# Optimization experiments

Hardware: AMD Instinct MI355X
Metric: run time of the kernel (lower is better)

The kernel has to match this reference:

```python
import jax, jax.numpy as jnp
import numpy as np

D = 1152      # hidden_size
H = 16        # num_heads
DH = D // H   # head_dim = 72
NCHUNK = 8    # images
L = 1024      # tokens per image (32x32 patches)
S = NCHUNK * L


def rotate_half(x):
    x1, x2 = jnp.split(x, 2, axis=-1)
    return jnp.concatenate([-x2, x1], axis=-1)


def setup_inputs() -> dict:
    key = jax.random.key(0)
    k0, k1, k2, k3, k4 = jax.random.split(key, 5)
    hidden_states = jax.random.normal(k0, (S, D), dtype=jnp.float32)
    qkv_w = jax.random.normal(k1, (3 * D, D), dtype=jnp.float32) * 0.02
    qkv_b = jax.random.normal(k2, (3 * D,), dtype=jnp.float32) * 0.02
    proj_w = jax.random.normal(k3, (D, D), dtype=jnp.float32) * 0.02
    proj_b = jax.random.normal(k4, (D,), dtype=jnp.float32) * 0.02
    # vision RoPE tables: [S, head_dim] with duplicated half-frequencies
    pos = jnp.arange(S, dtype=jnp.float32)
    inv_freq = 1.0 / (10000.0 ** (jnp.arange(0, DH, 2, dtype=jnp.float32) / DH))
    freqs = jnp.outer(pos, inv_freq)              # [S, DH//2]
    emb = jnp.concatenate([freqs, freqs], -1)     # [S, DH]
    cos, sin = jnp.cos(emb), jnp.sin(emb)
    cu_seqlens = jnp.arange(NCHUNK + 1, dtype=jnp.int32) * L
    return dict(hidden_states=hidden_states, cos=cos, sin=sin,
                qkv_w=qkv_w, qkv_b=qkv_b, proj_w=proj_w, proj_b=proj_b,
                cu_seqlens=cu_seqlens)


def reference(hidden_states, cos, sin, qkv_w, qkv_b, proj_w, proj_b, cu_seqlens):
    seq = hidden_states.shape[0]
    num_heads = H
    head_dim = qkv_w.shape[0] // (3 * num_heads)
    # fused QKV projection (torch Linear: x @ W^T + b)
    qkv = hidden_states @ qkv_w.T + qkv_b                 # [S, 3D]
    qkv = qkv.reshape(seq, 3, num_heads, head_dim)
    q, k, v = qkv[:, 0], qkv[:, 1], qkv[:, 2]             # [S, H, DH]
    # RoPE in fp32, broadcast cos/sin over heads
    c = cos[:, None, :].astype(jnp.float32)
    s = sin[:, None, :].astype(jnp.float32)
    qf, kf = q.astype(jnp.float32), k.astype(jnp.float32)
    q = (qf * c + rotate_half(qf) * s).astype(q.dtype)
    k = (kf * c + rotate_half(kf) * s).astype(k.dtype)
    # cu_seqlens defines equal-length segments -> vectorize over chunks
    cu = np.asarray(cu_seqlens)
    chunk = int(cu[1] - cu[0])
    n = seq // chunk
    qc = q.reshape(n, chunk, num_heads, head_dim)
    kc = k.reshape(n, chunk, num_heads, head_dim)
    vc = v.reshape(n, chunk, num_heads, head_dim)
    scale = head_dim ** -0.5
    attn = jnp.einsum('nqhd,nkhd->nhqk', qc, kc) * scale  # [n,H,L,L]
    attn = jax.nn.softmax(attn.astype(jnp.float32), axis=-1).astype(q.dtype)
    out = jnp.einsum('nhqk,nkhd->nqhd', attn, vc)         # [n,L,H,DH]
    out = out.reshape(seq, num_heads * head_dim)
    return out @ proj_w.T + proj_b
```

## Files before the change

### kernel.cpp

```cpp
#include <hip/hip_runtime.h>
#include <stdint.h>

typedef unsigned short ushort_t;
typedef short bf16x8 __attribute__((ext_vector_type(8)));
typedef float f32x4 __attribute__((ext_vector_type(4)));
typedef ushort_t us2 __attribute__((ext_vector_type(2)));
typedef ushort_t us4 __attribute__((ext_vector_type(4)));
typedef ushort_t us8 __attribute__((ext_vector_type(8)));

__device__ __forceinline__ float b2f(ushort_t u) {
    union { unsigned int i; float f; } v; v.i = ((unsigned int)u) << 16; return v.f;
}
__device__ __forceinline__ ushort_t f2b(float f) {
    union { float f; unsigned int i; } v; v.f = f;
    unsigned int r = v.i + 0x7fffu + ((v.i >> 16) & 1u);
    return (ushort_t)(r >> 16);
}

typedef __attribute__((address_space(3))) unsigned int lds_u32;
typedef __attribute__((address_space(1))) const unsigned int gbl_u32;

__device__ __forceinline__ void gload_lds16(const void* g, void* l) {
    __builtin_amdgcn_global_load_lds((gbl_u32*)g, (lds_u32*)l, 16, 0, 0);
}

__global__ void cvt_f32_bf16(const float* __restrict__ src, ushort_t* __restrict__ dst, int n8)
{
    const int i = blockIdx.x * 256 + threadIdx.x;
    if (i >= n8) return;
    f32x4 a = *(const f32x4*)&src[i * 8];
    f32x4 b = *(const f32x4*)&src[i * 8 + 4];
    us8 o;
#pragma unroll
    for (int j = 0; j < 4; j++) { o[j] = f2b(a[j]); o[j + 4] = f2b(b[j]); }
    *(us8*)&dst[i * 8] = o;
}

template <bool OUT_F32>
__global__ __launch_bounds__(256, 4) void gemm_bt_bias(
    const ushort_t* __restrict__ A, const ushort_t* __restrict__ B,
    const float* __restrict__ bias, void* __restrict__ Cv,
    int M, int N, int K)
{
    __shared__ short Sm[16384];

    const int t = threadIdx.x;
    const int lane = t & 63, w = t >> 6;
    const int qd = lane >> 4, ln = lane & 15;
    const int wm = w >> 1, wn = w & 1;
    const int m0 = blockIdx.y * 128, n0 = blockIdx.x * 128;
    const int KITER = K >> 5;

    f32x4 acc[4][4];
#pragma unroll
    for (int i = 0; i < 4; i++)
#pragma unroll
        for (int j = 0; j < 4; j++) acc[i][j] = (f32x4){0.f, 0.f, 0.f, 0.f};

    const int rA = t >> 2;
    const int colSw = ((t & 3) ^ ((rA >> 1) & 3)) * 8;
    const ushort_t* gA  = A + (size_t)(m0 + rA) * K + colSw;
    const ushort_t* gA2 = A + (size_t)(m0 + 64 + rA) * K + colSw;
    const ushort_t* gB  = B + (size_t)(n0 + rA) * K + colSw;
    const ushort_t* gB2 = B + (size_t)(n0 + 64 + rA) * K + colSw;

    gload_lds16(gA,  Sm + t * 8);
    gload_lds16(gA2, Sm + (t + 256) * 8);
    gload_lds16(gB,  Sm + 8192 + t * 8);
    gload_lds16(gB2, Sm + 8192 + (t + 256) * 8);

    const int pc = (qd ^ ((ln >> 1) & 3)) * 8;

    for (int kt = 0; kt < KITER; kt++) {
        __syncthreads();
        if (kt + 1 < KITER) {
            const int k1 = (kt + 1) << 5;
            const int nbo = ((kt + 1) & 1) * 4096;
            gload_lds16(gA + k1,  Sm + nbo + t * 8);
            gload_lds16(gA2 + k1, Sm + nbo + (t + 256) * 8);
            gload_lds16(gB + k1,  Sm + 8192 + nbo + t * 8);
            gload_lds16(gB2 + k1, Sm + 8192 + nbo + (t + 256) * 8);
        }
        const int cbo = (kt & 1) * 4096;
        const short* AsB = Sm + cbo;
        const short* BsB = Sm + 8192 + cbo;

        bf16x8 af[4], bfv[4];
#pragma unroll
        for (int i = 0; i < 4; i++)
            af[i] = *(const bf16x8*)&AsB[(wm * 64 + i * 16 + ln) * 32 + pc];
#pragma unroll
        for (int j = 0; j < 4; j++)
            bfv[j] = *(const bf16x8*)&BsB[(wn * 64 + j * 16 + ln) * 32 + pc];
#pragma unroll
        for (int i = 0; i < 4; i++)
#pragma unroll
            for (int j = 0; j < 4; j++)
                acc[i][j] = __builtin_amdgcn_mfma_f32_16x16x32_bf16(
                    af[i], bfv[j], acc[i][j], 0, 0, 0);
    }

    float bv[4];
#pragma unroll
    for (int j = 0; j < 4; j++) bv[j] = bias[n0 + wn * 64 + j * 16 + ln];

    if (!OUT_F32) {
        __syncthreads();
        ushort_t* Ct = (ushort_t*)Cv;
#pragma unroll
        for (int i = 0; i < 4; i++)
#pragma unroll
            for (int j = 0; j < 4; j++)
#pragma unroll
                for (int r = 0; r < 4; r++)
                    Sm[(wm * 64 + i * 16 + qd * 4 + r) * 128 + wn * 64 + j * 16 + ln] =
                        (short)f2b(acc[i][j][r] + bv[j]);
        __syncthreads();
#pragma unroll
        for (int q = 0; q < 8; q++) {
            const int c = t + q * 256;
            const int row = c >> 4, cc = c & 15;
            *(us8*)&Ct[(size_t)(m0 + row) * N + n0 + cc * 8] =
                *(const us8*)&Sm[row * 128 + cc * 8];
        }
    } else {
        float* Ct = (float*)Cv;
        float* Cf = (float*)Sm;
#pragma unroll
        for (int p = 0; p < 2; p++) {
            __syncthreads();
            if (wm == p) {
#pragma unroll
                for (int i = 0; i < 4; i++)
#pragma unroll
                    for (int j = 0; j < 4; j++)
#pragma unroll
                        for (int r = 0; r < 4; r++)
                            Cf[(i * 16 + qd * 4 + r) * 128 + wn * 64 + j * 16 + ln] =
                                acc[i][j][r] + bv[j];
            }
            __syncthreads();
#pragma unroll
            for (int q = 0; q < 8; q++) {
                const int c = t + q * 256;
                const int row = c >> 5, cc = c & 31;
                *(f32x4*)&Ct[(size_t)(m0 + p * 64 + row) * N + n0 + cc * 4] =
                    *(const f32x4*)&Cf[row * 128 + cc * 4];
            }
        }
    }
}

__global__ void rope_qk(ushort_t* __restrict__ qkv,
                        const float* __restrict__ cosb,
                        const float* __restrict__ sinb,
                        ushort_t* __restrict__ kb)
{
    const int idx = blockIdx.x * 256 + threadIdx.x;
    const int d0c = idx % 9;
    const int h = (idx / 9) & 15;
    const int s = idx / 144;
    const int d0 = d0c * 4;
    const int n = s >> 10, l = s & 1023;
    const size_t src = (size_t)s * 3456 + h * 72;
    const size_t dstrow = ((size_t)(n * 16 + h) * 1024 + l) * 128;

    f32x4 c1 = *(const f32x4*)&cosb[s * 72 + d0];
    f32x4 c2 = *(const f32x4*)&cosb[s * 72 + d0 + 36];
    f32x4 s1 = *(const f32x4*)&sinb[s * 72 + d0];
    f32x4 s2 = *(const f32x4*)&sinb[s * 72 + d0 + 36];

    {
        us4 x1 = *(const us4*)&qkv[src + d0];
        us4 x2 = *(const us4*)&qkv[src + d0 + 36];
        us4 o1, o2;
#pragma unroll
        for (int j = 0; j < 4; j++) {
            float a = b2f(x1[j]), b = b2f(x2[j]);
            o1[j] = f2b(a * c1[j] - b * s1[j]);
            o2[j] = f2b(b * c2[j] + a * s2[j]);
        }
        *(us4*)&qkv[src + d0] = o1;
        *(us4*)&qkv[src + d0 + 36] = o2;
    }
    {
        us4 x1 = *(const us4*)&qkv[src + 1152 + d0];
        us4 x2 = *(const us4*)&qkv[src + 1152 + d0 + 36];
        us4 o1, o2;
#pragma unroll
        for (int j = 0; j < 4; j++) {
            float a = b2f(x1[j]), b = b2f(x2[j]);
            o1[j] = f2b(a * c1[j] - b * s1[j]);
            o2[j] = f2b(b * c2[j] + a * s2[j]);
        }
        *(us4*)&kb[dstrow + d0] = o1;
        *(us4*)&kb[dstrow + d0 + 36] = o2;
    }
    if (d0c < 7) {
        us8 z = (us8){0, 0, 0, 0, 0, 0, 0, 0};
        *(us8*)&kb[dstrow + 72 + d0c * 8] = z;
    }
}

__global__ void v_transpose(const ushort_t* __restrict__ qkv, ushort_t* __restrict__ vt)
{
    __shared__ short T[64 * 80];
    const int t = threadIdx.x;
    const int nh = blockIdx.x >> 4, kvb = blockIdx.x & 15;
    const int h = nh & 15, n = nh >> 4;
    const int s0 = n * 1024 + kvb * 64;

#pragma unroll
    for (int i = 0; i < 3; i++) {
        int c = t + i * 256;
        if (c < 576) {
            int row = c / 9, off = (c % 9) * 8;
            *(us8*)&T[row * 80 + off] =
                *(const us8*)&qkv[(size_t)(s0 + row) * 3456 + 2304 + h * 72 + off];
        }
    }
    __syncthreads();

#pragma unroll
    for (int i = 0; i < 3; i++) {
        int c = t + i * 256;
        if (c < 640) {
            int d = c >> 3, kc = c & 7;
            us8 o;
            if (d < 72) {
#pragma unroll
                for (int j = 0; j < 8; j++) o[j] = (ushort_t)T[(kc * 8 + j) * 80 + d];
            } else {
                o = (us8){0, 0, 0, 0, 0, 0, 0, 0};
            }
            *(us8*)&vt[((size_t)nh * 80 + d) * 1024 + kvb * 64 + kc * 8] = o;
        }
    }
}

__global__ __launch_bounds__(256, 2) void flash_attn(
    const ushort_t* __restrict__ qkv, const ushort_t* __restrict__ kb,
    const ushort_t* __restrict__ vt, ushort_t* __restrict__ ob)
{
    __shared__ short Ks[2][32 * 128];
    __shared__ short VtS[2][80 * 32];
    __shared__ short Ps[4][64 * 40];

    const int t = threadIdx.x;
    const int lane = t & 63, w = t >> 6;
    const int qd = lane >> 4, ln = lane & 15;
    const int lnx = ln & 7;
    const int lns = (ln >> 1) & 3;
    const int nh = blockIdx.x >> 2, qt = blockIdx.x & 3;
    const int q0 = qt * 256;
    const int h = nh & 15, n = nh >> 4;
    const float scale = 0.11785113019775793f;

    const ushort_t* kbase = kb + (size_t)nh * 1024 * 128;
    const ushort_t* vbase = vt + (size_t)nh * 80 * 1024;

    bf16x8 qf[4][3];
    {
        const ushort_t* qsrc = qkv + (size_t)(n * 1024 + q0 + w * 64) * 3456 + h * 72;
#pragma unroll
        for (int im = 0; im < 4; im++)
#pragma unroll
            for (int ks = 0; ks < 3; ks++)
                qf[im][ks] = *(const bf16x8*)&qsrc[(size_t)(im * 16 + ln) * 3456 + ks * 32 + qd * 8];
    }

#pragma unroll
    for (int i = 0; i < 2; i++) {
        int c = t + i * 256, r = c >> 4, kc = c & 15;
        gload_lds16(kbase + (size_t)r * 128 + (kc ^ (r & 7)) * 8, &Ks[0][c * 8]);
    }
    {
        int c = t, d = c >> 2, kc = c & 3;
        gload_lds16(vbase + (size_t)d * 1024 + (kc ^ ((d >> 1) & 3)) * 8, &VtS[0][c * 8]);
        if (t < 64) {
            int c2 = t + 256, d2 = c2 >> 2, kc2 = c2 & 3;
            gload_lds16(vbase + (size_t)d2 * 1024 + (kc2 ^ ((d2 >> 1) & 3)) * 8, &VtS[0][c2 * 8]);
        }
    }

    float l_lane[4][4];
    f32x4 acc_o[4][5];
#pragma unroll
    for (int im = 0; im < 4; im++) {
#pragma unroll
        for (int r = 0; r < 4; r++) l_lane[im][r] = 0.f;
#pragma unroll
        for (int jn = 0; jn < 5; jn++) acc_o[im][jn] = (f32x4){0.f, 0.f, 0.f, 0.f};
    }

    for (int it = 0; it < 32; it++) {
        __syncthreads();

        if (it < 31) {
            const int nb = (it + 1) & 1;
            const ushort_t* knext = kbase + (size_t)(it + 1) * 4096;
#pragma unroll
            for (int i = 0; i < 2; i++) {
                int c = t + i * 256, r = c >> 4, kc = c & 15;
                gload_lds16(knext + (size_t)r * 128 + (kc ^ (r & 7)) * 8, &Ks[nb][c * 8]);
            }
            const ushort_t* vnext = vbase + (it + 1) * 32;
            {
                int c = t, d = c >> 2, kc = c & 3;
                gload_lds16(vnext + (size_t)d * 1024 + (kc ^ ((d >> 1) & 3)) * 8, &VtS[nb][c * 8]);
                if (t < 64) {
                    int c2 = t + 256, d2 = c2 >> 2, kc2 = c2 & 3;
                    gload_lds16(vnext + (size_t)d2 * 1024 + (kc2 ^ ((d2 >> 1) & 3)) * 8, &VtS[nb][c2 * 8]);
                }
            }
        }

        const short* KsB = Ks[it & 1];
        const short* VtB = VtS[it & 1];

        f32x4 sc[4][2];
#pragma unroll
        for (int im = 0; im < 4; im++)
#pragma unroll
            for (int jk = 0; jk < 2; jk++) sc[im][jk] = (f32x4){0.f, 0.f, 0.f, 0.f};
#pragma unroll
        for (int ks = 0; ks < 3; ks++) {
            const int m = ks * 4 + qd;
#pragma unroll
            for (int jk = 0; jk < 2; jk++) {
                bf16x8 bfr = *(const bf16x8*)&KsB[(jk * 16 + ln) * 128 + (m ^ lnx) * 8];
#pragma unroll
                for (int im = 0; im < 4; im++)
                    sc[im][jk] = __builtin_amdgcn_mfma_f32_16x16x32_bf16(
                        qf[im][ks], bfr, sc[im][jk], 0, 0, 0);
            }
        }

#pragma unroll
        for (int im = 0; im < 4; im++) {
#pragma unroll
            for (int r = 0; r < 4; r++) {
                float p0 = __expf(sc[im][0][r] * scale);
                float p1 = __expf(sc[im][1][r] * scale);
                l_lane[im][r] += p0 + p1;
                short* pd = &Ps[w][(im * 16 + qd * 4 + r) * 40 + ln];
                pd[0]  = (short)f2b(p0);
                pd[16] = (short)f2b(p1);
            }
        }

#pragma unroll
        for (int jn = 0; jn < 5; jn++) {
            bf16x8 vf = *(const bf16x8*)&VtB[(jn * 16 + ln) * 32 + (qd ^ lns) * 8];
#pragma unroll
            for (int im = 0; im < 4; im++) {
                bf16x8 pf = *(const bf16x8*)&Ps[w][(im * 16 + ln) * 40 + qd * 8];
                acc_o[im][jn] = __builtin_amdgcn_mfma_f32_16x16x32_bf16(
                    pf, vf, acc_o[im][jn], 0, 0, 0);
            }
        }
    }

    const size_t obase = ((size_t)(n * 1024 + q0 + w * 64)) * 1152 + h * 72;
#pragma unroll
    for (int im = 0; im < 4; im++) {
#pragma unroll
        for (int r = 0; r < 4; r++) {
            float l = l_lane[im][r];
            l += __shfl_xor(l, 1);
            l += __shfl_xor(l, 2);
            l += __shfl_xor(l, 4);
            l += __shfl_xor(l, 8);
            const float inv = 1.0f / l;
            const int rowl = im * 16 + qd * 4 + r;
#pragma unroll
            for (int jn = 0; jn < 5; jn++) {
                const int d = jn * 16 + ln;
                if (d < 72)
                    ob[obase + (size_t)rowl * 1152 + d] = f2b(acc_o[im][jn][r] * inv);
            }
        }
    }
}

extern "C" void kernel_launch(void* const* d_in, const int* in_sizes, int n_in,
                              void* d_out, int out_size, void* d_ws, size_t ws_size,
                              hipStream_t stream)
{
    const float* hs     = (const float*)d_in[0];
    const float* cosb   = (const float*)d_in[1];
    const float* sinb   = (const float*)d_in[2];
    const float* qkv_w  = (const float*)d_in[3];
    const float* qkv_b  = (const float*)d_in[4];
    const float* proj_w = (const float*)d_in[5];
    const float* proj_b = (const float*)d_in[6];

    char* ws = (char*)d_ws;
    ushort_t* hs_bf   = (ushort_t*)(ws);
    ushort_t* attn    = (ushort_t*)(ws);
    ushort_t* qkvw_bf = (ushort_t*)(ws + 18874368);
    ushort_t* projw_bf= (ushort_t*)(ws + 26836992);
    ushort_t* qkv_tmp = (ushort_t*)(ws + 29491200);
    ushort_t* k_buf   = (ushort_t*)(ws + 86114304);
    ushort_t* v_t     = (ushort_t*)(ws + 119668736);
    float*    out     = (float*)d_out;

    cvt_f32_bf16<<<4608, 256, 0, stream>>>(hs, hs_bf, 9437184 / 8);
    cvt_f32_bf16<<<1944, 256, 0, stream>>>(qkv_w, qkvw_bf, 3981312 / 8);
    cvt_f32_bf16<<<648, 256, 0, stream>>>(proj_w, projw_bf, 1327104 / 8);

    gemm_bt_bias<false><<<dim3(27, 64), 256, 0, stream>>>(hs_bf, qkvw_bf, qkv_b, qkv_tmp, 8192, 3456, 1152);
    rope_qk<<<4608, 256, 0, stream>>>(qkv_tmp, cosb, sinb, k_buf);
    v_transpose<<<2048, 256, 0, stream>>>(qkv_tmp, v_t);
    flash_attn<<<512, 256, 0, stream>>>(qkv_tmp, k_buf, v_t, attn);
    gemm_bt_bias<true><<<dim3(9, 64), 256, 0, stream>>>(attn, projw_bf, proj_b, out, 8192, 1152, 1152);
}
```

Measured before the change: 354.9 us.

## Replace QKV projection GEMM with 256x256-tile pipelined MFMA kernel

Adds a new 512-thread GEMM kernel that computes 256x256 output tiles for the QKV projection, replacing the 128x128 version. It uses 64-wide K steps with double-buffered LDS filled by direct global-to-LDS loads, XOR-swizzled LDS layouts, an XCD-aware block-index swizzle, and s_setprio around the MFMA bursts. The epilogue stages the bf16 output through LDS so global stores are coalesced. The goal is more data reuse per tile and less global and LDS traffic. In exchange it uses 128KB of LDS per block, launches only 448 blocks, and computes a padded N tile whose rows read past the weight matrix into the next workspace buffer.

Result: faster. 339.2 us (-4.4%).

```diff
diff --git a/kernel.cpp b/kernel.cpp
--- a/kernel.cpp
+++ b/kernel.cpp
@@ -34,6 +34,166 @@
 #pragma unroll
     for (int j = 0; j < 4; j++) { o[j] = f2b(a[j]); o[j + 4] = f2b(b[j]); }
     *(us8*)&dst[i * 8] = o;
+}
+
+__global__ __launch_bounds__(512, 2) void gemm256_bt_bias(
+    const ushort_t* __restrict__ A, const ushort_t* __restrict__ B,
+    const float* __restrict__ bias, ushort_t* __restrict__ C,
+    int K, int Npitch, int Nvalid)
+{
+    __shared__ short Sm[65536];
+
+    const int t = threadIdx.x;
+    const int lane = t & 63, w = t >> 6;
+    const int qd = lane >> 4, ln = lane & 15;
+    const int wm = w >> 2, wn = w & 3;
+
+    const int nwgx = gridDim.x;
+    const int bid = blockIdx.y * nwgx + blockIdx.x;
+    const int q8 = (nwgx * gridDim.y) >> 3;
+    const int swz = (bid & 7) * q8 + (bid >> 3);
+    const int m0 = (swz / nwgx) * 256, n0 = (swz % nwgx) * 256;
+
+    const int NT = K >> 6;
+    const int H4 = K >> 4;
+
+    const int sr = t >> 3, sc = t & 7;
+    const int csw = (sc ^ (sr & 7)) * 8;
+    const ushort_t* pA = A + (size_t)(m0 + sr) * K + csw;
+    const ushort_t* pB = B + (size_t)(n0 + sr) * K + csw;
+    const size_t rowK64 = (size_t)64 * K;
+    const size_t rowK128 = (size_t)128 * K;
+
+    auto stage = [&](int h) {
+        if (h >= H4) return;
+        const int ktt = h >> 2, reg = h & 3;
+        const ushort_t* s0;
+        int lo;
+        if (reg == 0)      { s0 = pB;           lo = 16384; }
+        else if (reg == 1) { s0 = pB + rowK128; lo = 24576; }
+        else if (reg == 2) { s0 = pA;           lo = 0;     }
+        else               { s0 = pA + rowK128; lo = 8192;  }
+        short* d = &Sm[(ktt & 1) * 32768 + lo + t * 8];
+        const ushort_t* g = s0 + (size_t)ktt * 64;
+        gload_lds16(g, d);
+        gload_lds16(g + rowK64, d + 4096);
+    };
+
+    f32x4 acc[8][4];
+#pragma unroll
+    for (int i = 0; i < 8; i++)
+#pragma unroll
+        for (int j = 0; j < 4; j++) acc[i][j] = (f32x4){0.f, 0.f, 0.f, 0.f};
+
+    const int pc0 = (qd ^ (ln & 7)) * 8;
+    const int pc1 = ((4 + qd) ^ (ln & 7)) * 8;
+    const int arow = wm * 128 + ln;
+    const int brow = wn * 64 + ln;
+
+#pragma unroll
+    for (int h = 0; h < 7; h++) stage(h);
+    asm volatile("s_waitcnt vmcnt(6)" ::: "memory");
+    __builtin_amdgcn_s_barrier();
+
+    for (int kt = 0; kt < NT; kt++) {
+        const int buf = (kt & 1) * 32768;
+        const short* Ab = &Sm[buf];
+        const short* Bb = &Sm[buf + 16384];
+        const int p = kt * 4;
+
+        bf16x8 a[8], bk0[4], bk1[4];
+
+#pragma unroll
+        for (int mf = 0; mf < 8; mf++)
+            a[mf] = *(const bf16x8*)&Ab[(arow + mf * 16) * 64 + pc0];
+#pragma unroll
+        for (int nf = 0; nf < 4; nf++) {
+            bk0[nf] = *(const bf16x8*)&Bb[(brow + nf * 16) * 64 + pc0];
+            bk1[nf] = *(const bf16x8*)&Bb[(brow + nf * 16) * 64 + pc1];
+        }
+        stage(p + 7);
+        __builtin_amdgcn_s_barrier();
+        asm volatile("s_waitcnt lgkmcnt(0)" ::: "memory");
+        __builtin_amdgcn_s_setprio(1);
+#pragma unroll
+        for (int mf = 0; mf < 8; mf++) {
+            acc[mf][0] = __builtin_amdgcn_mfma_f32_16x16x32_bf16(a[mf], bk0[0], acc[mf][0], 0, 0, 0);
+            acc[mf][1] = __builtin_amdgcn_mfma_f32_16x16x32_bf16(a[mf], bk0[1], acc[mf][1], 0, 0, 0);
+        }
+        __builtin_amdgcn_s_setprio(0);
+        __builtin_amdgcn_s_barrier();
+
+        stage(p + 8);
+        __builtin_amdgcn_s_barrier();
+        asm volatile("s_waitcnt lgkmcnt(0)" ::: "memory");
+        __builtin_amdgcn_s_setprio(1);
+#pragma unroll
+        for (int mf = 0; mf < 8; mf++) {
+            acc[mf][2] = __builtin_amdgcn_mfma_f32_16x16x32_bf16(a[mf], bk0[2], acc[mf][2], 0, 0, 0);
+            acc[mf][3] = __builtin_amdgcn_mfma_f32_16x16x32_bf16(a[mf], bk0[3], acc[mf][3], 0, 0, 0);
+        }
+        __builtin_amdgcn_s_setprio(0);
+        __builtin_amdgcn_s_barrier();
+
+#pragma unroll
+        for (int mf = 0; mf < 8; mf++)
+            a[mf] = *(const bf16x8*)&Ab[(arow + mf * 16) * 64 + pc1];
+        stage(p + 9);
+        __builtin_amdgcn_s_barrier();
+        asm volatile("s_waitcnt lgkmcnt(0)" ::: "memory");
+        __builtin_amdgcn_s_setprio(1);
+#pragma unroll
+        for (int mf = 0; mf < 8; mf++) {
+            acc[mf][0] = __builtin_amdgcn_mfma_f32_16x16x32_bf16(a[mf], bk1[0], acc[mf][0], 0, 0, 0);
+            acc[mf][1] = __builtin_amdgcn_mfma_f32_16x16x32_bf16(a[mf], bk1[1], acc[mf][1], 0, 0, 0);
+        }
+        __builtin_amdgcn_s_setprio(0);
+        __builtin_amdgcn_s_barrier();
+
+        stage(p + 10);
+        __builtin_amdgcn_s_barrier();
+        asm volatile("s_waitcnt lgkmcnt(0)" ::: "memory");
+        __builtin_amdgcn_s_setprio(1);
+#pragma unroll
+        for (int mf = 0; mf < 8; mf++) {
+            acc[mf][2] = __builtin_amdgcn_mfma_f32_16x16x32_bf16(a[mf], bk1[2], acc[mf][2], 0, 0, 0);
+            acc[mf][3] = __builtin_amdgcn_mfma_f32_16x16x32_bf16(a[mf], bk1[3], acc[mf][3], 0, 0, 0);
+        }
+        __builtin_amdgcn_s_setprio(0);
+        if (kt < NT - 2) { asm volatile("s_waitcnt vmcnt(6)" ::: "memory"); }
+        else             { asm volatile("s_waitcnt vmcnt(0)" ::: "memory"); }
+        __builtin_amdgcn_s_barrier();
+    }
+
+    __syncthreads();
+    float bv[4];
+#pragma unroll
+    for (int nf = 0; nf < 4; nf++) {
+        const int gc = n0 + wn * 64 + nf * 16 + ln;
+        bv[nf] = (gc < Nvalid) ? bias[gc] : 0.f;
+    }
+    char* Smb = (char*)Sm;
+#pragma unroll
+    for (int mf = 0; mf < 8; mf++) {
+        const int row = wm * 128 + mf * 16 + qd * 4;
+#pragma unroll
+        for (int nf = 0; nf < 4; nf++) {
+            const int swc = ((wn * 64 + nf * 16 + ln) * 2) ^ (qd << 5);
+#pragma unroll
+            for (int r = 0; r < 4; r++)
+                *(ushort_t*)(Smb + (row + r) * 512 + swc) = f2b(acc[mf][nf][r] + bv[nf]);
+        }
+    }
+    __syncthreads();
+#pragma unroll
+    for (int q = 0; q < 16; q++) {
+        const int s = t + q * 512;
+        const int row = s >> 5, c8 = s & 31;
+        const int gcol = n0 + c8 * 8;
+        if (gcol < Nvalid)
+            *(us8*)&C[(size_t)(m0 + row) * Npitch + gcol] =
+                *(const us8*)(Smb + row * 512 + ((c8 * 16) ^ (((row >> 2) & 3) << 5)));
+    }
 }
 
 template <bool OUT_F32>
@@ -409,7 +569,7 @@
     cvt_f32_bf16<<<1944, 256, 0, stream>>>(qkv_w, qkvw_bf, 3981312 / 8);
     cvt_f32_bf16<<<648, 256, 0, stream>>>(proj_w, projw_bf, 1327104 / 8);
 
-    gemm_bt_bias<false><<<dim3(27, 64), 256, 0, stream>>>(hs_bf, qkvw_bf, qkv_b, qkv_tmp, 8192, 3456, 1152);
+    gemm256_bt_bias<<<dim3(14, 32), 512, 0, stream>>>(hs_bf, qkvw_bf, qkv_b, qkv_tmp, 1152, 3456, 3456);
     rope_qk<<<4608, 256, 0, stream>>>(qkv_tmp, cosb, sinb, k_buf);
     v_transpose<<<2048, 256, 0, stream>>>(qkv_tmp, v_t);
     flash_attn<<<512, 256, 0, stream>>>(qkv_tmp, k_buf, v_t, attn);
```
